# Performance work log

Measured on AMD Instinct MI355X. Metric: run time of the kernel, lower is better.

Reference implementation:

```python
import jax, jax.numpy as jnp
import numpy as np
import math

H = 16          # num_attention_heads
D = 64          # attention_head_size
MAX_POS = 1024  # max_position_embeddings


def setup_inputs() -> dict:
    key = jax.random.key(0)
    ks = jax.random.split(key, 6)
    B, S, HID = 4, 1024, 1024
    scale = 1.0 / math.sqrt(HID)
    return {
        "hidden_states": jax.random.normal(ks[0], (B, S, HID), jnp.float32),
        "attention_mask": jnp.zeros((B, 1, 1, S), jnp.float32),
        "Wq": jax.random.normal(ks[1], (HID, HID), jnp.float32) * scale,
        "bq": jnp.zeros((HID,), jnp.float32),
        "Wk": jax.random.normal(ks[2], (HID, HID), jnp.float32) * scale,
        "bk": jnp.zeros((HID,), jnp.float32),
        "Wv": jax.random.normal(ks[3], (HID, HID), jnp.float32) * scale,
        "bv": jnp.zeros((HID,), jnp.float32),
        "dist_emb": jax.random.normal(ks[4], (2 * MAX_POS - 1, D), jnp.float32) * 0.02,
    }


def _split_heads(x):
    # [B,S,H*D] -> [B,H,S,D]
    B, S, _ = x.shape
    return x.reshape(B, S, H, D).transpose(0, 2, 1, 3)


def reference(hidden_states, attention_mask, Wq, bq, Wk, bk, Wv, bv, dist_emb):
    B, S, _ = hidden_states.shape
    q = _split_heads(hidden_states @ Wq.T + bq)   # [B,H,S,D]
    k = _split_heads(hidden_states @ Wk.T + bk)
    v = _split_heads(hidden_states @ Wv.T + bv)

    scores = jnp.einsum("bhqd,bhkd->bhqk", q, k)  # [B,H,S,S]

    # relative_key_query positional bias
    pos_l = jnp.arange(S)[:, None]
    pos_r = jnp.arange(S)[None, :]
    distance = pos_l - pos_r + (MAX_POS - 1)      # [S,S] in [0, 2*MAX_POS-2]
    pos_emb = dist_emb[distance]                  # [S,S,D]
    rel_q = jnp.einsum("bhld,lrd->bhlr", q, pos_emb)
    rel_k = jnp.einsum("bhrd,lrd->bhlr", k, pos_emb)
    scores = (scores + rel_q + rel_k) / math.sqrt(D)

    scores = scores + attention_mask
    probs = jax.nn.softmax(scores, axis=-1)
    ctx = jnp.einsum("bhqk,bhkd->bhqd", probs, v)  # [B,H,S,D]
    ctx = ctx.transpose(0, 2, 1, 3).reshape(B, S, H * D)
    return ctx
```

## Files before the change

### kernel.cpp

```cpp
#include <hip/hip_runtime.h>
#include <hip/hip_bf16.h>

#define B_   4
#define S_   1024
#define HID_ 1024
#define H_   16
#define D_   64

typedef __attribute__((ext_vector_type(4))) float f32x4;
typedef __attribute__((ext_vector_type(8))) __bf16 bf16v8;
typedef __attribute__((ext_vector_type(8))) unsigned short u16x8;

#define MFMA16(a, b, c) __builtin_amdgcn_mfma_f32_16x16x32_bf16((a), (b), (c), 0, 0, 0)
#define GLOAD16(gp, lp)                                                              \
    __builtin_amdgcn_global_load_lds((const __attribute__((address_space(1))) void*)(gp), \
                                     (__attribute__((address_space(3))) void*)(lp), 16, 0, 0)

__device__ __forceinline__ unsigned short f2bs_hw(float f) {
    __bf16 h = (__bf16)f;
    return __builtin_bit_cast(unsigned short, h);
}
__device__ __forceinline__ unsigned pack2bf(float a, float b) {
    unsigned short lo = f2bs_hw(a), hi = f2bs_hw(b);
    return (unsigned)lo | ((unsigned)hi << 16);
}
__device__ __forceinline__ float bs2f(unsigned short s) {
    union { unsigned u; float f; } v; v.u = ((unsigned)s) << 16;
    return v.f;
}

__global__ void conv_e_kernel(const float* __restrict__ E, unsigned short* __restrict__ Eb) {
    int i = (blockIdx.x * 256 + threadIdx.x) * 4;
    const int n = 2047 * 64;
    if (i + 3 < n) {
        float4 x = *(const float4*)(E + i);
        Eb[i + 0] = f2bs_hw(x.x); Eb[i + 1] = f2bs_hw(x.y);
        Eb[i + 2] = f2bs_hw(x.z); Eb[i + 3] = f2bs_hw(x.w);
    } else {
        for (int k = i; k < n; ++k) Eb[k] = f2bs_hw(E[k]);
    }
}

__global__ __launch_bounds__(256)
void proj_kernel(const float* __restrict__ X,
                 const float* __restrict__ Wq, const float* __restrict__ bq,
                 const float* __restrict__ Wk, const float* __restrict__ bk,
                 const float* __restrict__ Wv, const float* __restrict__ bv,
                 unsigned short* __restrict__ Qo, unsigned short* __restrict__ Ko,
                 unsigned short* __restrict__ Vo)
{
    __shared__ unsigned short Al[128][40];
    __shared__ unsigned short Bl[128][40];

    const int tile = blockIdx.x;
    const int rt = tile / 24, ct = tile % 24;
    const int row0 = rt * 128, col0 = ct * 128;
    const int which = col0 >> 10;
    const float* Wm   = (which == 0) ? Wq : (which == 1) ? Wk : Wv;
    const float* bias = (which == 0) ? bq : (which == 1) ? bk : bv;
    unsigned short* Out = (which == 0) ? Qo : (which == 1) ? Ko : Vo;
    const int oc0 = col0 & 1023;

    const int t = threadIdx.x;
    const int lane = t & 63, wv = t >> 6;
    const int wr = wv >> 1, wc = wv & 1;
    const int lg = lane >> 4, lc = lane & 15;

    f32x4 acc[4][4] = {};

    for (int k0 = 0; k0 < 1024; k0 += 32) {
        __syncthreads();
#pragma unroll
        for (int l = 0; l < 4; ++l) {
            int idx = l * 256 + t;
            int r = idx >> 3, kq = (idx & 7) * 4;
            float4 a = *(const float4*)(X  + (size_t)(row0 + r) * 1024 + k0 + kq);
            float4 b = *(const float4*)(Wm + (size_t)(oc0  + r) * 1024 + k0 + kq);
            short4 as, bs;
            as.x = (short)f2bs_hw(a.x); as.y = (short)f2bs_hw(a.y);
            as.z = (short)f2bs_hw(a.z); as.w = (short)f2bs_hw(a.w);
            bs.x = (short)f2bs_hw(b.x); bs.y = (short)f2bs_hw(b.y);
            bs.z = (short)f2bs_hw(b.z); bs.w = (short)f2bs_hw(b.w);
            *(short4*)&Al[r][kq] = as;
            *(short4*)&Bl[r][kq] = bs;
        }
        __syncthreads();
        bf16v8 af[4], bfg[4];
#pragma unroll
        for (int m = 0; m < 4; ++m) af[m]  = *(const bf16v8*)&Al[wr * 64 + m * 16 + lc][lg * 8];
#pragma unroll
        for (int n = 0; n < 4; ++n) bfg[n] = *(const bf16v8*)&Bl[wc * 64 + n * 16 + lc][lg * 8];
#pragma unroll
        for (int m = 0; m < 4; ++m)
#pragma unroll
            for (int n = 0; n < 4; ++n)
                acc[m][n] = MFMA16(af[m], bfg[n], acc[m][n]);
    }

#pragma unroll
    for (int m = 0; m < 4; ++m)
#pragma unroll
        for (int n = 0; n < 4; ++n) {
            int j = oc0 + wc * 64 + n * 16 + lc;
            int hh = j >> 6, dd = j & 63;
            float bv_ = bias[j];
#pragma unroll
            for (int r = 0; r < 4; ++r) {
                int i = row0 + wr * 64 + m * 16 + lg * 4 + r;
                int bb = i >> 10, ss = i & 1023;
                float v = acc[m][n][r] + bv_;
                Out[((size_t)(bb * 16 + hh) * 1024 + ss) * 64 + dd] = f2bs_hw(v);
            }
        }
}

__global__ __launch_bounds__(256)
void attn_kernel(const unsigned short* __restrict__ Q,
                 const unsigned short* __restrict__ K,
                 const unsigned short* __restrict__ V,
                 const float* __restrict__ mask,
                 const unsigned short* __restrict__ Eb,
                 float* __restrict__ Out)
{
    __shared__ __align__(16) unsigned short Kl[64][64];
    __shared__ __align__(16) unsigned short El[128][64];
    __shared__ __align__(16) unsigned short VTl[64][72];
    __shared__ __align__(16) unsigned short QDl[4][16][136];
    __shared__ __align__(16) unsigned short KDl[64][132];
    __shared__ __align__(16) unsigned Pex[4 * 16 * 36];
    __shared__ float maskl[64];

    const int t = threadIdx.x;
    const int lane = t & 63, w = t >> 6;
    const int lg = lane >> 4, lc = lane & 15;

    const int bid = blockIdx.x;
    const int bh = bid & 63;
    const int qt = bid >> 6;
    const int b = bh >> 4, h = bh & 15;
    const int i0 = qt * 64;
    const int i_loc = w * 16 + lc;

    const float C2 = 0.125f * 1.44269504089f;
    const float L2E = 1.44269504089f;

    const unsigned short* Qh = Q + (size_t)bh * S_ * D_;
    const unsigned short* Kh = K + (size_t)bh * S_ * D_;
    const unsigned short* Vh = V + (size_t)bh * S_ * D_;

    bf16v8 qf[2];
#pragma unroll
    for (int ks = 0; ks < 2; ++ks)
        qf[ks] = *(const bf16v8*)(Qh + (size_t)(i0 + i_loc) * D_ + ks * 32 + lg * 8);

    u16x8 ones_u;
#pragma unroll
    for (int e = 0; e < 8; ++e) ones_u[e] = 0x3F80;
    const bf16v8 onesf = __builtin_bit_cast(bf16v8, ones_u);

    float m_r = -1e30f;
    f32x4 lacc = (f32x4){0.f, 0.f, 0.f, 0.f};
    f32x4 ctx[4];
#pragma unroll
    for (int nd = 0; nd < 4; ++nd) ctx[nd] = (f32x4){0.f, 0.f, 0.f, 0.f};

    unsigned* PexW = &Pex[(w * 16 + lc) * 36];

    for (int jt = 0; jt < 16; ++jt) {
        const int j0 = jt * 64;
        const int dbase = i0 - j0 + 960;
        __syncthreads();

#pragma unroll
        for (int l = 0; l < 2; ++l) {
            int idx = l * 256 + t;
            int r = idx >> 3, su = idx & 7;
            int u = su ^ (r & 7);
            GLOAD16(Kh + (size_t)(j0 + r) * 64 + u * 8,
                    &Kl[0][0] + (size_t)(l * 256 + w * 64) * 8);
        }
        {
            int a = t & 7, rb = (t >> 3) << 1;
            int cq = a * 8;
            u16x8 v0 = *(const u16x8*)(Vh + (size_t)(j0 + rb) * 64 + cq);
            u16x8 v1 = *(const u16x8*)(Vh + (size_t)(j0 + rb + 1) * 64 + cq);
            int jst = (rb + (a << 3)) & 63;
#pragma unroll
            for (int e = 0; e < 8; ++e)
                *(unsigned*)&VTl[cq + e][jst] = (unsigned)v0[e] | ((unsigned)v1[e] << 16);
        }
        if (jt == 0) {
            const int sb0 = dbase & 127;
#pragma unroll
            for (int l = 0; l < 4; ++l) {
                int idx = l * 256 + t;
                int sl = idx >> 3, su = idx & 7;
                int u = su ^ (sl & 7);
                int dr = dbase + ((sl - sb0) & 127);
                if (dr > 2046) dr = 2046;
                GLOAD16(Eb + (size_t)dr * 64 + u * 8,
                        &El[0][0] + (size_t)(l * 256 + w * 64) * 8);
            }
        } else {
            const int sb = dbase & 127;
#pragma unroll
            for (int l = 0; l < 2; ++l) {
                int idx = l * 256 + t;
                int rl = idx >> 3, su = idx & 7;
                int u = su ^ (rl & 7);
                GLOAD16(Eb + (size_t)(dbase + rl) * 64 + u * 8,
                        &El[sb][0] + (size_t)(l * 256 + w * 64) * 8);
            }
        }
        if (t < 64) maskl[t] = mask[(size_t)b * S_ + j0 + t] * L2E;
        __syncthreads();

        bf16v8 kfa[2];
#pragma unroll
        for (int ks = 0; ks < 2; ++ks) {
            int u = (ks * 4 + lg) ^ (lc & 7);
            kfa[ks] = *(const bf16v8*)&Kl[w * 16 + lc][u * 8];
        }
        __builtin_amdgcn_s_setprio(1);
#pragma unroll
        for (int nd = 0; nd < 8; ++nd) {
            f32x4 kd = (f32x4){0.f, 0.f, 0.f, 0.f};
            int sl = (dbase + nd * 16 + lc) & 127;
#pragma unroll
            for (int ks = 0; ks < 2; ++ks) {
                int u = (ks * 4 + lg) ^ (lc & 7);
                bf16v8 ef = *(const bf16v8*)&El[sl][u * 8];
                kd = MFMA16(ef, kfa[ks], kd);
            }
            uint2 pk;
            pk.x = pack2bf(kd[0], kd[1]);
            pk.y = pack2bf(kd[2], kd[3]);
            *(uint2*)&KDl[w * 16 + lc][nd * 16 + lg * 4] = pk;
        }
#pragma unroll
        for (int nd = 0; nd < 4; ++nd) {
            f32x4 qd = (f32x4){0.f, 0.f, 0.f, 0.f};
            int sl = (dbase + nd * 16 + lc) & 127;
#pragma unroll
            for (int ks = 0; ks < 2; ++ks) {
                int u = (ks * 4 + lg) ^ (lc & 7);
                bf16v8 ef = *(const bf16v8*)&El[sl][u * 8];
                qd = MFMA16(ef, qf[ks], qd);
            }
            int slot0 = ((dbase & 127) + nd * 16 + lg * 4) & 127;
            uint2 pk;
            pk.x = pack2bf(qd[0], qd[1]);
            pk.y = pack2bf(qd[2], qd[3]);
            *(uint2*)&QDl[w][lc][slot0] = pk;
        }
        if (jt == 0) {
#pragma unroll
            for (int nd = 4; nd < 8; ++nd) {
                f32x4 qd = (f32x4){0.f, 0.f, 0.f, 0.f};
                int sl = (dbase + nd * 16 + lc) & 127;
#pragma unroll
                for (int ks = 0; ks < 2; ++ks) {
                    int u = (ks * 4 + lg) ^ (lc & 7);
                    bf16v8 ef = *(const bf16v8*)&El[sl][u * 8];
                    qd = MFMA16(ef, qf[ks], qd);
                }
                int slot0 = ((dbase & 127) + nd * 16 + lg * 4) & 127;
                uint2 pk;
                pk.x = pack2bf(qd[0], qd[1]);
                pk.y = pack2bf(qd[2], qd[3]);
                *(uint2*)&QDl[w][lc][slot0] = pk;
            }
        }
        __builtin_amdgcn_s_setprio(0);
        __syncthreads();

        f32x4 s[4];
#pragma unroll
        for (int n = 0; n < 4; ++n) {
            s[n] = (f32x4){0.f, 0.f, 0.f, 0.f};
#pragma unroll
            for (int ks = 0; ks < 2; ++ks) {
                int u = (ks * 4 + lg) ^ (lc & 7);
                bf16v8 kb = *(const bf16v8*)&Kl[n * 16 + lc][u * 8];
                s[n] = MFMA16(kb, qf[ks], s[n]);
            }
        }

        const unsigned short* QDw = &QDl[w][lc][0];
        float vmax = -1e30f;
#pragma unroll
        for (int n = 0; n < 4; ++n) {
            int jb = n * 16 + lg * 4;
            float4 mk = *(const float4*)&maskl[jb];
            int kbase = jb * 131 + i_loc + 63;
            int qbase = dbase + i_loc - jb + 63;
#pragma unroll
            for (int r = 0; r < 4; ++r) {
                float qdv = bs2f(QDw[(qbase - r) & 127]);
                float kdv = bs2f((&KDl[0][0])[kbase + 131 * r]);
                float mkr = (r == 0) ? mk.x : (r == 1) ? mk.y : (r == 2) ? mk.z : mk.w;
                float val = (s[n][r] + qdv + kdv) * C2 + mkr;
                s[n][r] = val;
                vmax = fmaxf(vmax, val);
            }
        }
        vmax = fmaxf(vmax, __shfl_xor(vmax, 16));
        vmax = fmaxf(vmax, __shfl_xor(vmax, 32));
        float mnew = fmaxf(m_r, vmax);
        float alpha = exp2f(m_r - mnew);
        m_r = mnew;

#pragma unroll
        for (int n = 0; n < 4; ++n)
#pragma unroll
            for (int r = 0; r < 4; ++r)
                s[n][r] = exp2f(s[n][r] - mnew);

#pragma unroll
        for (int r = 0; r < 4; ++r) lacc[r] *= alpha;
#pragma unroll
        for (int nd = 0; nd < 4; ++nd)
#pragma unroll
            for (int r = 0; r < 4; ++r)
                ctx[nd][r] *= alpha;

#pragma unroll
        for (int n = 0; n < 4; ++n) {
            uint2 pk;
            pk.x = pack2bf(s[n][0], s[n][1]);
            pk.y = pack2bf(s[n][2], s[n][3]);
            *(uint2*)&PexW[n * 8 + lg * 2] = pk;
        }
        bf16v8 pfB[2];
#pragma unroll
        for (int ks = 0; ks < 2; ++ks) {
            int nc = 2 * ks + (lg >> 1);
            pfB[ks] = *(const bf16v8*)&PexW[nc * 8 + (lg & 1) * 4];
        }

        __builtin_amdgcn_s_setprio(1);
        lacc = MFMA16(onesf, pfB[0], lacc);
        lacc = MFMA16(onesf, pfB[1], lacc);
#pragma unroll
        for (int nd = 0; nd < 4; ++nd) {
            int vrow = nd * 16 + lc;
#pragma unroll
            for (int ks = 0; ks < 2; ++ks) {
                int jst = (ks * 32 + lg * 8 + ((vrow >> 3) << 3)) & 63;
                bf16v8 vf = *(const bf16v8*)&VTl[vrow][jst];
                ctx[nd] = MFMA16(vf, pfB[ks], ctx[nd]);
            }
        }
        __builtin_amdgcn_s_setprio(0);
    }

    float inv = 1.0f / lacc[0];
    float* outp = Out + ((size_t)(b * S_ + i0 + i_loc) * H_ + h) * D_;
#pragma unroll
    for (int nd = 0; nd < 4; ++nd) {
        float4 o;
        o.x = ctx[nd][0] * inv;
        o.y = ctx[nd][1] * inv;
        o.z = ctx[nd][2] * inv;
        o.w = ctx[nd][3] * inv;
        *(float4*)(outp + nd * 16 + lg * 4) = o;
    }
}

extern "C" void kernel_launch(void* const* d_in, const int* in_sizes, int n_in,
                              void* d_out, int out_size, void* d_ws, size_t ws_size,
                              hipStream_t stream)
{
    const float* X    = (const float*)d_in[0];
    const float* mask = (const float*)d_in[1];
    const float* Wq   = (const float*)d_in[2];
    const float* bq   = (const float*)d_in[3];
    const float* Wk   = (const float*)d_in[4];
    const float* bk   = (const float*)d_in[5];
    const float* Wv   = (const float*)d_in[6];
    const float* bv   = (const float*)d_in[7];
    const float* E    = (const float*)d_in[8];
    float* Out = (float*)d_out;

    const size_t headN = (size_t)B_ * H_ * S_ * D_;
    unsigned short* Qw = (unsigned short*)d_ws;
    unsigned short* Kw = Qw + headN;
    unsigned short* Vw = Kw + headN;
    unsigned short* Ebw = Vw + headN;

    conv_e_kernel<<<dim3(128), dim3(256), 0, stream>>>(E, Ebw);
    proj_kernel<<<dim3(768), dim3(256), 0, stream>>>(X, Wq, bq, Wk, bk, Wv, bv, Qw, Kw, Vw);
    attn_kernel<<<dim3(1024), dim3(256), 0, stream>>>(Qw, Kw, Vw, mask, Ebw, Out);
}
```

Measured before the change: 167.2 us.

## Pre-convert X and weights to bf16, use async LDS loads in projection, skip rescale

Adds separate conversion kernels that cast X and the Q/K/V weights to bf16 in the workspace. The projection GEMM then loads bf16 tiles straight into swizzled LDS with global_load_lds, uses K-steps of 64, and remaps block indices to group tiles. In the attention kernel the position-embedding fragment loads are shared between the K and Q distance MFMAs, and the online-softmax rescale is skipped when no lane's max grows. The extra conversion launches add memory traffic and launch overhead in exchange for a cheaper GEMM inner loop.

```diff
diff --git a/kernel.cpp b/kernel.cpp
--- a/kernel.cpp
+++ b/kernel.cpp
@@ -29,72 +29,85 @@
     return v.f;
 }
 
-__global__ void conv_e_kernel(const float* __restrict__ E, unsigned short* __restrict__ Eb) {
-    int i = (blockIdx.x * 256 + threadIdx.x) * 4;
-    const int n = 2047 * 64;
-    if (i + 3 < n) {
-        float4 x = *(const float4*)(E + i);
-        Eb[i + 0] = f2bs_hw(x.x); Eb[i + 1] = f2bs_hw(x.y);
-        Eb[i + 2] = f2bs_hw(x.z); Eb[i + 3] = f2bs_hw(x.w);
-    } else {
-        for (int k = i; k < n; ++k) Eb[k] = f2bs_hw(E[k]);
+__global__ void conv_kernel(const float* __restrict__ src, unsigned short* __restrict__ dst,
+                            int n4) {
+    int i = blockIdx.x * 256 + threadIdx.x;
+    int stride = gridDim.x * 256;
+    for (; i < n4; i += stride) {
+        float4 x = *(const float4*)(src + (size_t)i * 4);
+        uint2 o;
+        o.x = pack2bf(x.x, x.y);
+        o.y = pack2bf(x.z, x.w);
+        *(uint2*)(dst + (size_t)i * 4) = o;
     }
 }
 
 __global__ __launch_bounds__(256)
-void proj_kernel(const float* __restrict__ X,
-                 const float* __restrict__ Wq, const float* __restrict__ bq,
-                 const float* __restrict__ Wk, const float* __restrict__ bk,
-                 const float* __restrict__ Wv, const float* __restrict__ bv,
+void proj_kernel(const unsigned short* __restrict__ Xb,
+                 const unsigned short* __restrict__ Wqb, const float* __restrict__ bq,
+                 const unsigned short* __restrict__ Wkb, const float* __restrict__ bk,
+                 const unsigned short* __restrict__ Wvb, const float* __restrict__ bv,
                  unsigned short* __restrict__ Qo, unsigned short* __restrict__ Ko,
                  unsigned short* __restrict__ Vo)
 {
-    __shared__ unsigned short Al[128][40];
-    __shared__ unsigned short Bl[128][40];
-
-    const int tile = blockIdx.x;
+    __shared__ __align__(16) unsigned short Al[128][64];
+    __shared__ __align__(16) unsigned short Bl[128][64];
+
+    const int bid = blockIdx.x;
+    const int tile = (bid & 7) * 96 + (bid >> 3);
     const int rt = tile / 24, ct = tile % 24;
     const int row0 = rt * 128, col0 = ct * 128;
     const int which = col0 >> 10;
-    const float* Wm   = (which == 0) ? Wq : (which == 1) ? Wk : Wv;
-    const float* bias = (which == 0) ? bq : (which == 1) ? bk : bv;
-    unsigned short* Out = (which == 0) ? Qo : (which == 1) ? Ko : Vo;
+    const unsigned short* Wm = (which == 0) ? Wqb : (which == 1) ? Wkb : Wvb;
+    const float* bias        = (which == 0) ? bq  : (which == 1) ? bk  : bv;
+    unsigned short* Out      = (which == 0) ? Qo  : (which == 1) ? Ko  : Vo;
     const int oc0 = col0 & 1023;
 
     const int t = threadIdx.x;
-    const int lane = t & 63, wv = t >> 6;
-    const int wr = wv >> 1, wc = wv & 1;
+    const int lane = t & 63, w = t >> 6;
+    const int wr = w >> 1, wc = w & 1;
     const int lg = lane >> 4, lc = lane & 15;
 
     f32x4 acc[4][4] = {};
 
-    for (int k0 = 0; k0 < 1024; k0 += 32) {
+    for (int k0 = 0; k0 < 1024; k0 += 64) {
         __syncthreads();
 #pragma unroll
         for (int l = 0; l < 4; ++l) {
             int idx = l * 256 + t;
-            int r = idx >> 3, kq = (idx & 7) * 4;
-            float4 a = *(const float4*)(X  + (size_t)(row0 + r) * 1024 + k0 + kq);
-            float4 b = *(const float4*)(Wm + (size_t)(oc0  + r) * 1024 + k0 + kq);
-            short4 as, bs;
-            as.x = (short)f2bs_hw(a.x); as.y = (short)f2bs_hw(a.y);
-            as.z = (short)f2bs_hw(a.z); as.w = (short)f2bs_hw(a.w);
-            bs.x = (short)f2bs_hw(b.x); bs.y = (short)f2bs_hw(b.y);
-            bs.z = (short)f2bs_hw(b.z); bs.w = (short)f2bs_hw(b.w);
-            *(short4*)&Al[r][kq] = as;
-            *(short4*)&Bl[r][kq] = bs;
-        }
-        __syncthreads();
-        bf16v8 af[4], bfg[4];
-#pragma unroll
-        for (int m = 0; m < 4; ++m) af[m]  = *(const bf16v8*)&Al[wr * 64 + m * 16 + lc][lg * 8];
-#pragma unroll
-        for (int n = 0; n < 4; ++n) bfg[n] = *(const bf16v8*)&Bl[wc * 64 + n * 16 + lc][lg * 8];
+            int r = idx >> 3, su = idx & 7;
+            int u = su ^ (r & 7);
+            GLOAD16(Xb + (size_t)(row0 + r) * 1024 + k0 + u * 8,
+                    &Al[0][0] + (size_t)(l * 256 + w * 64) * 8);
+            GLOAD16(Wm + (size_t)(oc0 + r) * 1024 + k0 + u * 8,
+                    &Bl[0][0] + (size_t)(l * 256 + w * 64) * 8);
+        }
+        __syncthreads();
+
+        bf16v8 af[4][2], bfg[4][2];
 #pragma unroll
         for (int m = 0; m < 4; ++m)
 #pragma unroll
-            for (int n = 0; n < 4; ++n)
-                acc[m][n] = MFMA16(af[m], bfg[n], acc[m][n]);
+            for (int ks = 0; ks < 2; ++ks) {
+                int u = (ks * 4 + lg) ^ (lc & 7);
+                af[m][ks] = *(const bf16v8*)&Al[wr * 64 + m * 16 + lc][u * 8];
+            }
+#pragma unroll
+        for (int n = 0; n < 4; ++n)
+#pragma unroll
+            for (int ks = 0; ks < 2; ++ks) {
+                int u = (ks * 4 + lg) ^ (lc & 7);
+                bfg[n][ks] = *(const bf16v8*)&Bl[wc * 64 + n * 16 + lc][u * 8];
+            }
+        __builtin_amdgcn_s_setprio(1);
+#pragma unroll
+        for (int m = 0; m < 4; ++m)
+#pragma unroll
+            for (int n = 0; n < 4; ++n) {
+                acc[m][n] = MFMA16(af[m][0], bfg[n][0], acc[m][n]);
+                acc[m][n] = MFMA16(af[m][1], bfg[n][1], acc[m][n]);
+            }
+        __builtin_amdgcn_s_setprio(0);
     }
 
 #pragma unroll
@@ -224,51 +237,27 @@
         __builtin_amdgcn_s_setprio(1);
 #pragma unroll
         for (int nd = 0; nd < 8; ++nd) {
+            int sl = (dbase + nd * 16 + lc) & 127;
+            int u0 = lg ^ (lc & 7);
+            int u1 = (4 + lg) ^ (lc & 7);
+            bf16v8 ef0 = *(const bf16v8*)&El[sl][u0 * 8];
+            bf16v8 ef1 = *(const bf16v8*)&El[sl][u1 * 8];
             f32x4 kd = (f32x4){0.f, 0.f, 0.f, 0.f};
-            int sl = (dbase + nd * 16 + lc) & 127;
-#pragma unroll
-            for (int ks = 0; ks < 2; ++ks) {
-                int u = (ks * 4 + lg) ^ (lc & 7);
-                bf16v8 ef = *(const bf16v8*)&El[sl][u * 8];
-                kd = MFMA16(ef, kfa[ks], kd);
-            }
+            kd = MFMA16(ef0, kfa[0], kd);
+            kd = MFMA16(ef1, kfa[1], kd);
             uint2 pk;
             pk.x = pack2bf(kd[0], kd[1]);
             pk.y = pack2bf(kd[2], kd[3]);
             *(uint2*)&KDl[w * 16 + lc][nd * 16 + lg * 4] = pk;
-        }
-#pragma unroll
-        for (int nd = 0; nd < 4; ++nd) {
-            f32x4 qd = (f32x4){0.f, 0.f, 0.f, 0.f};
-            int sl = (dbase + nd * 16 + lc) & 127;
-#pragma unroll
-            for (int ks = 0; ks < 2; ++ks) {
-                int u = (ks * 4 + lg) ^ (lc & 7);
-                bf16v8 ef = *(const bf16v8*)&El[sl][u * 8];
-                qd = MFMA16(ef, qf[ks], qd);
-            }
-            int slot0 = ((dbase & 127) + nd * 16 + lg * 4) & 127;
-            uint2 pk;
-            pk.x = pack2bf(qd[0], qd[1]);
-            pk.y = pack2bf(qd[2], qd[3]);
-            *(uint2*)&QDl[w][lc][slot0] = pk;
-        }
-        if (jt == 0) {
-#pragma unroll
-            for (int nd = 4; nd < 8; ++nd) {
+            if (nd < 4 || jt == 0) {
                 f32x4 qd = (f32x4){0.f, 0.f, 0.f, 0.f};
-                int sl = (dbase + nd * 16 + lc) & 127;
-#pragma unroll
-                for (int ks = 0; ks < 2; ++ks) {
-                    int u = (ks * 4 + lg) ^ (lc & 7);
-                    bf16v8 ef = *(const bf16v8*)&El[sl][u * 8];
-                    qd = MFMA16(ef, qf[ks], qd);
-                }
+                qd = MFMA16(ef0, qf[0], qd);
+                qd = MFMA16(ef1, qf[1], qd);
                 int slot0 = ((dbase & 127) + nd * 16 + lg * 4) & 127;
-                uint2 pk;
-                pk.x = pack2bf(qd[0], qd[1]);
-                pk.y = pack2bf(qd[2], qd[3]);
-                *(uint2*)&QDl[w][lc][slot0] = pk;
+                uint2 qk2;
+                qk2.x = pack2bf(qd[0], qd[1]);
+                qk2.y = pack2bf(qd[2], qd[3]);
+                *(uint2*)&QDl[w][lc][slot0] = qk2;
             }
         }
         __builtin_amdgcn_s_setprio(0);
@@ -306,23 +295,25 @@
         }
         vmax = fmaxf(vmax, __shfl_xor(vmax, 16));
         vmax = fmaxf(vmax, __shfl_xor(vmax, 32));
-        float mnew = fmaxf(m_r, vmax);
-        float alpha = exp2f(m_r - mnew);
-        m_r = mnew;
+
+        if (__any(vmax > m_r)) {
+            float mnew = fmaxf(m_r, vmax);
+            float alpha = exp2f(m_r - mnew);
+            m_r = mnew;
+#pragma unroll
+            for (int r = 0; r < 4; ++r) lacc[r] *= alpha;
+#pragma unroll
+            for (int nd = 0; nd < 4; ++nd)
+#pragma unroll
+                for (int r = 0; r < 4; ++r)
+                    ctx[nd][r] *= alpha;
+        }
 
 #pragma unroll
         for (int n = 0; n < 4; ++n)
 #pragma unroll
             for (int r = 0; r < 4; ++r)
-                s[n][r] = exp2f(s[n][r] - mnew);
-
-#pragma unroll
-        for (int r = 0; r < 4; ++r) lacc[r] *= alpha;
-#pragma unroll
-        for (int nd = 0; nd < 4; ++nd)
-#pragma unroll
-            for (int r = 0; r < 4; ++r)
-                ctx[nd][r] *= alpha;
+                s[n][r] = exp2f(s[n][r] - m_r);
 
 #pragma unroll
         for (int n = 0; n < 4; ++n) {
@@ -383,12 +374,20 @@
     float* Out = (float*)d_out;
 
     const size_t headN = (size_t)B_ * H_ * S_ * D_;
-    unsigned short* Qw = (unsigned short*)d_ws;
-    unsigned short* Kw = Qw + headN;
-    unsigned short* Vw = Kw + headN;
+    unsigned short* Qw  = (unsigned short*)d_ws;
+    unsigned short* Kw  = Qw + headN;
+    unsigned short* Vw  = Kw + headN;
     unsigned short* Ebw = Vw + headN;
-
-    conv_e_kernel<<<dim3(128), dim3(256), 0, stream>>>(E, Ebw);
-    proj_kernel<<<dim3(768), dim3(256), 0, stream>>>(X, Wq, bq, Wk, bk, Wv, bv, Qw, Kw, Vw);
+    unsigned short* Xb  = Ebw + (size_t)2047 * 64;
+    unsigned short* Wqb = Xb + (size_t)4096 * 1024;
+    unsigned short* Wkb = Wqb + (size_t)1024 * 1024;
+    unsigned short* Wvb = Wkb + (size_t)1024 * 1024;
+
+    conv_kernel<<<dim3(128),  dim3(256), 0, stream>>>(E,  Ebw, 2047 * 64 / 4);
+    conv_kernel<<<dim3(2048), dim3(256), 0, stream>>>(X,  Xb,  4096 * 1024 / 4);
+    conv_kernel<<<dim3(1024), dim3(256), 0, stream>>>(Wq, Wqb, 1024 * 1024 / 4);
+    conv_kernel<<<dim3(1024), dim3(256), 0, stream>>>(Wk, Wkb, 1024 * 1024 / 4);
+    conv_kernel<<<dim3(1024), dim3(256), 0, stream>>>(Wv, Wvb, 1024 * 1024 / 4);
+    proj_kernel<<<dim3(768), dim3(256), 0, stream>>>(Xb, Wqb, bq, Wkb, bk, Wvb, bv, Qw, Kw, Vw);
     attn_kernel<<<dim3(1024), dim3(256), 0, stream>>>(Qw, Kw, Vw, mask, Ebw, Out);
 }
```

Measured after the change: 167.6 us. No clear change (+0.2%).
